# Optimization experiments

Hardware: AMD Instinct MI355X
Metric: run time of the kernel (lower is better)

The kernel has to match this reference:

```python
import jax, jax.numpy as jnp
import numpy as np

B, S, D, H = 2, 2048, 1024, 16
DK = D // H


def setup_inputs() -> dict:
    key = jax.random.key(0)
    ks = jax.random.split(key, 7)
    q = jax.random.normal(ks[0], (B, S, D), dtype=jnp.float32)
    k = jax.random.normal(ks[1], (B, S, D), dtype=jnp.float32)
    v = jax.random.normal(ks[2], (B, S, D), dtype=jnp.float32)
    # causal mask (1 = keep, 0 = mask) broadcast over batch/heads
    mask = jnp.tril(jnp.ones((S, S), dtype=jnp.int32))[None, None, :, :]
    scale = 1.0 / np.sqrt(DK)
    W_q = jax.random.normal(ks[3], (D, D), dtype=jnp.float32) * 0.02
    W_k = jax.random.normal(ks[4], (D, D), dtype=jnp.float32) * 0.02
    W_v = jax.random.normal(ks[5], (D, D), dtype=jnp.float32) * 0.02
    W_o = jax.random.normal(ks[6], (D, D), dtype=jnp.float32) * 0.02
    return {"q": q, "k": k, "v": v, "mask": mask,
            "W_q": W_q, "W_k": W_k, "W_v": W_v, "W_o": W_o}


def _split_heads(x):
    # [B, S, D] -> [B, H, S, DK]
    b, s, _ = x.shape
    return x.reshape(b, s, H, DK).transpose(0, 2, 1, 3)


def reference(q, k, v, mask, W_q, W_k, W_v, W_o):
    # nn.Linear(bias=False): y = x @ W.T
    qh = _split_heads(q @ W_q.T)
    kh = _split_heads(k @ W_k.T)
    vh = _split_heads(v @ W_v.T)
    scores = jnp.einsum("bhqd,bhkd->bhqk", qh, kh) / np.sqrt(DK)
    scores = jnp.where(mask == 0, jnp.float32(-1e9), scores)
    attn = jax.nn.softmax(scores, axis=-1)  # dropout p=0 -> identity
    out = jnp.einsum("bhqk,bhkd->bhqd", attn, vh)
    out = out.transpose(0, 2, 1, 3).reshape(q.shape[0], q.shape[1], D)
    return out @ W_o.T
```

## Files before the change

kernel.cpp:

```cpp
#include <hip/hip_runtime.h>
#include <stdint.h>
#include <stddef.h>

typedef __bf16 bf16;
typedef __attribute__((ext_vector_type(4))) __bf16 bf16x4;
typedef __attribute__((ext_vector_type(8))) __bf16 bf16x8;
typedef __attribute__((ext_vector_type(4))) float floatx4;

#define NB 2
#define NS 2048
#define ND 1024
#define NH 16
#define NDK 64
#define NBH (NB*NH)
#define NBS (NB*NS)

__device__ inline void gl2lds16(const void* g, void* l) {
  __builtin_amdgcn_global_load_lds(
      (const __attribute__((address_space(1))) uint32_t*)(const uint32_t*)g,
      (__attribute__((address_space(3))) uint32_t*)(uint32_t*)l,
      16, 0, 0);
}

__global__ __launch_bounds__(256)
void convert_w3(const float* __restrict__ Wq, const float* __restrict__ Wk,
                const float* __restrict__ Wv, bf16* __restrict__ Wb)
{
  const int z = blockIdx.y;
  const float* src = (z == 0) ? Wq : (z == 1) ? Wk : Wv;
  bf16* dst = Wb + (size_t)z * (ND * ND);
  const size_t off = ((size_t)blockIdx.x * 256 + threadIdx.x) * 32;
#pragma unroll
  for (int c = 0; c < 2; c++) {
    bf16x8 o[2];
#pragma unroll
    for (int h = 0; h < 2; h++) {
      const float4 a = *(const float4*)(src + off + c * 16 + h * 8);
      const float4 b = *(const float4*)(src + off + c * 16 + h * 8 + 4);
      o[h][0] = (bf16)a.x; o[h][1] = (bf16)a.y; o[h][2] = (bf16)a.z; o[h][3] = (bf16)a.w;
      o[h][4] = (bf16)b.x; o[h][5] = (bf16)b.y; o[h][6] = (bf16)b.z; o[h][7] = (bf16)b.w;
    }
    *(bf16x8*)(dst + off + c * 16) = o[0];
    *(bf16x8*)(dst + off + c * 16 + 8) = o[1];
  }
}

__global__ __launch_bounds__(256)
void convert_w1(const float* __restrict__ src, bf16* __restrict__ dst)
{
  const size_t off = ((size_t)blockIdx.x * 256 + threadIdx.x) * 32;
#pragma unroll
  for (int c = 0; c < 2; c++) {
    bf16x8 o[2];
#pragma unroll
    for (int h = 0; h < 2; h++) {
      const float4 a = *(const float4*)(src + off + c * 16 + h * 8);
      const float4 b = *(const float4*)(src + off + c * 16 + h * 8 + 4);
      o[h][0] = (bf16)a.x; o[h][1] = (bf16)a.y; o[h][2] = (bf16)a.z; o[h][3] = (bf16)a.w;
      o[h][4] = (bf16)b.x; o[h][5] = (bf16)b.y; o[h][6] = (bf16)b.z; o[h][7] = (bf16)b.w;
    }
    *(bf16x8*)(dst + off + c * 16) = o[0];
    *(bf16x8*)(dst + off + c * 16 + 8) = o[1];
  }
}

__global__ __launch_bounds__(256)
void proj_gemm(const float* __restrict__ q, const float* __restrict__ k,
               const float* __restrict__ v, const bf16* __restrict__ Wb,
               bf16* __restrict__ Qh, bf16* __restrict__ Kh,
               bf16* __restrict__ Vt)
{
  const int z = blockIdx.y, bx = blockIdx.x;
  const int tid = threadIdx.x;
  const int wave = tid >> 6, lane = tid & 63;
  const int quad = lane >> 4, l15 = lane & 15;

  const float* X = (z == 0) ? q : (z == 1) ? k : v;
  const bf16* W = Wb + (size_t)z * (ND * ND);
  const int c = bx & 7, r = bx >> 3;
  const int m0 = (c * 4 + (r >> 3)) * 128, n0 = (r & 7) * 128;

  __shared__ float Af[2][128 * 32];
  __shared__ bf16  Bs[2][128 * 32];

  const int wm = (wave >> 1) * 64, wn = (wave & 1) * 64;

  floatx4 acc[4][4];
#pragma unroll
  for (int i = 0; i < 4; i++)
#pragma unroll
    for (int j = 0; j < 4; j++) acc[i][j] = (floatx4)(0.0f);

  auto stage = [&](int kt, int buf) {
    const int k0 = kt * 32;
#pragma unroll
    for (int it = 0; it < 4; it++) {
      const int lin = it * 256 + tid;
      const int row = lin >> 3, slot = lin & 7;
      const int srcCh = slot ^ (row & 7);
      gl2lds16(X + (size_t)(m0 + row) * ND + k0 + srcCh * 4,
               Af[buf] + row * 32 + slot * 4);
    }
#pragma unroll
    for (int it = 0; it < 2; it++) {
      const int lin = it * 256 + tid;
      const int row = lin >> 2, ch = lin & 3;
      gl2lds16(W + (size_t)(n0 + row) * ND + k0 + ch * 8,
               Bs[buf] + lin * 8);
    }
  };

  stage(0, 0);
  for (int kk = 0; kk < 32; kk++) {
    const int cur = kk & 1;
    __builtin_amdgcn_s_waitcnt(0);
    __syncthreads();
    if (kk + 1 < 32) stage(kk + 1, cur ^ 1);

    bf16x8 af[4], bfr[4];
#pragma unroll
    for (int i = 0; i < 4; i++) {
      const int rl = wm + i * 16 + l15, r7 = rl & 7;
      const float* Ab = Af[cur] + rl * 32;
      const float4 p0 = *(const float4*)(Ab + (((2 * quad) ^ r7) << 2));
      const float4 p1 = *(const float4*)(Ab + (((2 * quad + 1) ^ r7) << 2));
      bf16x8 a;
      a[0] = (bf16)p0.x; a[1] = (bf16)p0.y; a[2] = (bf16)p0.z; a[3] = (bf16)p0.w;
      a[4] = (bf16)p1.x; a[5] = (bf16)p1.y; a[6] = (bf16)p1.z; a[7] = (bf16)p1.w;
      af[i] = a;
    }
#pragma unroll
    for (int j = 0; j < 4; j++)
      bfr[j] = *(const bf16x8*)(Bs[cur] + (wn + j * 16 + l15) * 32 + quad * 8);
#pragma unroll
    for (int i = 0; i < 4; i++)
#pragma unroll
      for (int j = 0; j < 4; j++)
        acc[i][j] = __builtin_amdgcn_mfma_f32_16x16x32_bf16(af[i], bfr[j],
                                                            acc[i][j], 0, 0, 0);
  }

  bf16* O = (z == 0) ? Qh : (z == 1) ? Kh : Vt;
#pragma unroll
  for (int i = 0; i < 4; i++) {
    const int rowb = m0 + wm + i * 16 + quad * 4;
#pragma unroll
    for (int j = 0; j < 4; j++) {
      const int col = n0 + wn + j * 16 + l15;
#pragma unroll
      for (int rr = 0; rr < 4; rr++) {
        const int row = rowb + rr;
        const bf16 o = (bf16)acc[i][j][rr];
        const int b = row >> 11, s = row & 2047;
        const int h = col >> 6,  dk = col & 63;
        if (z < 2)
          O[(((size_t)(b * NH + h)) * NS + s) * NDK + dk] = o;
        else
          O[(((size_t)(b * NH + h)) * NDK + dk) * NS + s] = o;
      }
    }
  }
}

__global__ __launch_bounds__(256)
void attn_fwd(const bf16* __restrict__ Qh, const bf16* __restrict__ Kh,
              const bf16* __restrict__ Vt, bf16* __restrict__ Ctx)
{
  const int x = blockIdx.x, bh = blockIdx.y;
  const int tid = threadIdx.x, wave = tid >> 6, lane = tid & 63;
  const int quad = lane >> 4, l15 = lane & 15;

  __shared__ bf16 Ks[2][64 * 64];
  __shared__ bf16 Vs[2][64 * 64];
  __shared__ bf16 Ps[4][16 * 64];

  const size_t qkb = (size_t)bh * NS * NDK;
  const size_t vb  = (size_t)bh * NDK * NS;
  const int b = bh >> 4, h = bh & 15;
  const float C = 0.125f * 1.44269504088896f;

  auto stage = [&](int kt, int buf) {
#pragma unroll
    for (int it = 0; it < 2; it++) {
      const int lin = it * 256 + tid;
      const int row = lin >> 3;
      const int chS = (lin & 7) ^ (row & 7);
      gl2lds16(Kh + qkb + (size_t)(kt * 64 + row) * NDK + chS * 8,
               Ks[buf] + lin * 8);
      gl2lds16(Vt + vb + (size_t)row * NS + kt * 64 + chS * 8,
               Vs[buf] + lin * 8);
    }
  };

  for (int ph = 0; ph < 2; ph++) {
    const int qt = ph ? x : 31 - x;
    const int qrow0 = qt * 64 + wave * 16;

    bf16x8 qf0, qf1;
    {
      const bf16* qp = Qh + qkb + (size_t)(qrow0 + l15) * NDK + quad * 8;
      qf0 = *(const bf16x8*)qp;
      qf1 = *(const bf16x8*)(qp + 32);
    }

    float lsum[4] = {0.0f, 0.0f, 0.0f, 0.0f};
    floatx4 oacc[4];
#pragma unroll
    for (int j = 0; j < 4; j++) oacc[j] = (floatx4)(0.0f);

    __syncthreads();
    stage(0, 0);

    for (int kt = 0; kt <= qt; kt++) {
      const int cur = kt & 1;
      __builtin_amdgcn_s_waitcnt(0);
      __syncthreads();
      if (kt < qt) stage(kt + 1, cur ^ 1);

      const bf16* Ksb = Ks[cur];
      const bf16* Vsb = Vs[cur];

      floatx4 sa[4];
#pragma unroll
      for (int jt = 0; jt < 4; jt++) {
        const int rr = jt * 16 + l15;
        const bf16x8 kf0 = *(const bf16x8*)(Ksb + rr * 64 + ((quad ^ (rr & 7)) << 3));
        const bf16x8 kf1 = *(const bf16x8*)(Ksb + rr * 64 + (((4 + quad) ^ (rr & 7)) << 3));
        floatx4 zz = (floatx4)(0.0f);
        zz = __builtin_amdgcn_mfma_f32_16x16x32_bf16(qf0, kf0, zz, 0, 0, 0);
        zz = __builtin_amdgcn_mfma_f32_16x16x32_bf16(qf1, kf1, zz, 0, 0, 0);
        sa[jt] = zz;
      }

      const bool diag = (kt == qt);
#pragma unroll
      for (int jt = 0; jt < 4; jt++) {
        const int col = jt * 16 + l15;
#pragma unroll
        for (int rr = 0; rr < 4; rr++) {
          const int row = quad * 4 + rr;
          float p = exp2f(sa[jt][rr] * C);
          if (diag) p = (kt * 64 + col <= qrow0 + row) ? p : 0.0f;
          lsum[rr] += p;
          Ps[wave][row * 64 + ((((col >> 3) ^ (row & 7))) << 3) + (col & 7)] =
              (bf16)p;
        }
      }

#pragma unroll
      for (int ks = 0; ks < 2; ks++) {
        const bf16x8 pf = *(const bf16x8*)(
            &Ps[wave][l15 * 64 + (((ks * 4 + quad) ^ (l15 & 7)) << 3)]);
#pragma unroll
        for (int jt = 0; jt < 4; jt++) {
          const int rr = jt * 16 + l15;
          const bf16x8 vf = *(const bf16x8*)(
              Vsb + rr * 64 + (((ks * 4 + quad) ^ (rr & 7)) << 3));
          oacc[jt] = __builtin_amdgcn_mfma_f32_16x16x32_bf16(pf, vf,
                                                             oacc[jt], 0, 0, 0);
        }
      }
    }

#pragma unroll
    for (int off = 1; off < 16; off <<= 1)
#pragma unroll
      for (int rr = 0; rr < 4; rr++) lsum[rr] += __shfl_xor(lsum[rr], off, 64);

#pragma unroll
    for (int jt = 0; jt < 4; jt++)
#pragma unroll
      for (int rr = 0; rr < 4; rr++) {
        const int srow = qrow0 + quad * 4 + rr;
        Ctx[((size_t)b * NS + srow) * ND + h * 64 + jt * 16 + l15] =
            (bf16)(oacc[jt][rr] / lsum[rr]);
      }
  }
}

__global__ __launch_bounds__(256)
void out_gemm(const bf16* __restrict__ Ctx, const bf16* __restrict__ WoB,
              float* __restrict__ out)
{
  const int bx = blockIdx.x, tid = threadIdx.x;
  const int wave = tid >> 6, lane = tid & 63;
  const int quad = lane >> 4, l15 = lane & 15;
  const int c = bx & 7, r = bx >> 3;
  const int m0 = (c * 8 + (r >> 3)) * 64, n0 = (r & 7) * 128;
  const int wm = (wave & 1) * 32, wn = (wave >> 1) * 64;

  __shared__ bf16 As[2][64 * 32];
  __shared__ bf16 Bs[2][128 * 32];

  floatx4 acc[2][4];
#pragma unroll
  for (int i = 0; i < 2; i++)
#pragma unroll
    for (int j = 0; j < 4; j++) acc[i][j] = (floatx4)(0.0f);

  auto stage = [&](int kt, int buf) {
    const int k0 = kt * 32;
    {
      const int row = tid >> 2, ch = tid & 3;
      gl2lds16(Ctx + (size_t)(m0 + row) * ND + k0 + ch * 8, As[buf] + tid * 8);
    }
#pragma unroll
    for (int it = 0; it < 2; it++) {
      const int lin = it * 256 + tid;
      const int row = lin >> 2, ch = lin & 3;
      gl2lds16(WoB + (size_t)(n0 + row) * ND + k0 + ch * 8, Bs[buf] + lin * 8);
    }
  };

  stage(0, 0);
  for (int kk = 0; kk < 32; kk++) {
    const int cur = kk & 1;
    __builtin_amdgcn_s_waitcnt(0);
    __syncthreads();
    if (kk + 1 < 32) stage(kk + 1, cur ^ 1);

    bf16x8 af[2], bfr[4];
#pragma unroll
    for (int i = 0; i < 2; i++)
      af[i] = *(const bf16x8*)(As[cur] + (wm + i * 16 + l15) * 32 + quad * 8);
#pragma unroll
    for (int j = 0; j < 4; j++)
      bfr[j] = *(const bf16x8*)(Bs[cur] + (wn + j * 16 + l15) * 32 + quad * 8);
#pragma unroll
    for (int i = 0; i < 2; i++)
#pragma unroll
      for (int j = 0; j < 4; j++)
        acc[i][j] = __builtin_amdgcn_mfma_f32_16x16x32_bf16(af[i], bfr[j],
                                                            acc[i][j], 0, 0, 0);
  }

#pragma unroll
  for (int i = 0; i < 2; i++) {
    const int rowb = m0 + wm + i * 16 + quad * 4;
#pragma unroll
    for (int j = 0; j < 4; j++) {
      const int col = n0 + wn + j * 16 + l15;
#pragma unroll
      for (int rr = 0; rr < 4; rr++)
        out[(size_t)(rowb + rr) * ND + col] = acc[i][j][rr];
    }
  }
}

extern "C" void kernel_launch(void* const* d_in, const int* in_sizes, int n_in,
                              void* d_out, int out_size, void* d_ws, size_t ws_size,
                              hipStream_t stream) {
  const float* q  = (const float*)d_in[0];
  const float* k  = (const float*)d_in[1];
  const float* v  = (const float*)d_in[2];
  const float* Wq = (const float*)d_in[4];
  const float* Wk = (const float*)d_in[5];
  const float* Wv = (const float*)d_in[6];
  const float* Wo = (const float*)d_in[7];
  float* out = (float*)d_out;

  const size_t elems = (size_t)NBS * ND;
  bf16* Qh  = (bf16*)d_ws;
  bf16* Kh  = Qh + elems;
  bf16* Vt  = Kh + elems;
  bf16* Ctx = Vt + elems;
  bf16* Wb  = Ctx;
  bf16* WoB = Vt;

  dim3 blk(256);
  convert_w3<<<dim3(128, 3), blk, 0, stream>>>(Wq, Wk, Wv, Wb);
  proj_gemm<<<dim3(256, 3), blk, 0, stream>>>(q, k, v, Wb, Qh, Kh, Vt);
  attn_fwd<<<dim3(16, NBH), blk, 0, stream>>>(Qh, Kh, Vt, Ctx);
  convert_w1<<<dim3(128), blk, 0, stream>>>(Wo, WoB);
  out_gemm<<<dim3(512), blk, 0, stream>>>(Ctx, WoB, out);
}
```

Before: 285.0 us.

## Replace direct global-to-LDS loads with register-staged prefetch in projection and output GEMMs

```diff
diff --git a/kernel.cpp b/kernel.cpp
--- a/kernel.cpp
+++ b/kernel.cpp
@@ -80,8 +80,11 @@
   const int c = bx & 7, r = bx >> 3;
   const int m0 = (c * 4 + (r >> 3)) * 128, n0 = (r & 7) * 128;
 
-  __shared__ float Af[2][128 * 32];
-  __shared__ bf16  Bs[2][128 * 32];
+  __shared__ bf16 As[128 * 32];
+  __shared__ bf16 Bs[128 * 32];
+
+  const int arow = tid >> 3, ach = tid & 7;
+  const int brow = tid >> 1, bch = tid & 1;
 
   const int wm = (wave >> 1) * 64, wn = (wave & 1) * 64;
 
@@ -91,47 +94,54 @@
 #pragma unroll
     for (int j = 0; j < 4; j++) acc[i][j] = (floatx4)(0.0f);
 
-  auto stage = [&](int kt, int buf) {
+  float4 ra[2][4];
+  bf16x8 rb[2];
+
+  auto loadA = [&](int kt, int p) {
     const int k0 = kt * 32;
 #pragma unroll
+    for (int it = 0; it < 4; it++)
+      ra[p][it] = *(const float4*)(X + (size_t)(m0 + it * 32 + arow) * ND + k0 + ach * 4);
+  };
+  auto loadB = [&](int kt) {
+    const int k0 = kt * 32;
+#pragma unroll
+    for (int it = 0; it < 2; it++) {
+      const int lin = it * 256 + tid;
+      const int row = lin >> 2, ch = lin & 3;
+      rb[it] = *(const bf16x8*)(W + (size_t)(n0 + row) * ND + k0 + ch * 8);
+    }
+  };
+
+  loadA(0, 0); loadB(0); loadA(1, 1);
+
+  for (int kk = 0; kk < 32; kk++) {
+    const int p = kk & 1;
+    __syncthreads();
+#pragma unroll
     for (int it = 0; it < 4; it++) {
-      const int lin = it * 256 + tid;
-      const int row = lin >> 3, slot = lin & 7;
-      const int srcCh = slot ^ (row & 7);
-      gl2lds16(X + (size_t)(m0 + row) * ND + k0 + srcCh * 4,
-               Af[buf] + row * 32 + slot * 4);
+      bf16x4 a;
+      a[0] = (bf16)ra[p][it].x; a[1] = (bf16)ra[p][it].y;
+      a[2] = (bf16)ra[p][it].z; a[3] = (bf16)ra[p][it].w;
+      *(bf16x4*)(As + (it * 32 + arow) * 32 + ach * 4) = a;
     }
 #pragma unroll
     for (int it = 0; it < 2; it++) {
       const int lin = it * 256 + tid;
       const int row = lin >> 2, ch = lin & 3;
-      gl2lds16(W + (size_t)(n0 + row) * ND + k0 + ch * 8,
-               Bs[buf] + lin * 8);
-    }
-  };
-
-  stage(0, 0);
-  for (int kk = 0; kk < 32; kk++) {
-    const int cur = kk & 1;
-    __builtin_amdgcn_s_waitcnt(0);
-    __syncthreads();
-    if (kk + 1 < 32) stage(kk + 1, cur ^ 1);
+      *(bf16x8*)(Bs + row * 32 + ch * 8) = rb[it];
+    }
+    __syncthreads();
+    if (kk + 2 < 32) loadA(kk + 2, p);
+    if (kk + 1 < 32) loadB(kk + 1);
 
     bf16x8 af[4], bfr[4];
 #pragma unroll
-    for (int i = 0; i < 4; i++) {
-      const int rl = wm + i * 16 + l15, r7 = rl & 7;
-      const float* Ab = Af[cur] + rl * 32;
-      const float4 p0 = *(const float4*)(Ab + (((2 * quad) ^ r7) << 2));
-      const float4 p1 = *(const float4*)(Ab + (((2 * quad + 1) ^ r7) << 2));
-      bf16x8 a;
-      a[0] = (bf16)p0.x; a[1] = (bf16)p0.y; a[2] = (bf16)p0.z; a[3] = (bf16)p0.w;
-      a[4] = (bf16)p1.x; a[5] = (bf16)p1.y; a[6] = (bf16)p1.z; a[7] = (bf16)p1.w;
-      af[i] = a;
-    }
+    for (int i = 0; i < 4; i++)
+      af[i] = *(const bf16x8*)(As + (wm + i * 16 + l15) * 32 + quad * 8);
 #pragma unroll
     for (int j = 0; j < 4; j++)
-      bfr[j] = *(const bf16x8*)(Bs[cur] + (wn + j * 16 + l15) * 32 + quad * 8);
+      bfr[j] = *(const bf16x8*)(Bs + (wn + j * 16 + l15) * 32 + quad * 8);
 #pragma unroll
     for (int i = 0; i < 4; i++)
 #pragma unroll
@@ -289,8 +299,10 @@
   const int m0 = (c * 8 + (r >> 3)) * 64, n0 = (r & 7) * 128;
   const int wm = (wave & 1) * 32, wn = (wave >> 1) * 64;
 
-  __shared__ bf16 As[2][64 * 32];
-  __shared__ bf16 Bs[2][128 * 32];
+  __shared__ bf16 As[64 * 32];
+  __shared__ bf16 Bs[128 * 32];
+
+  const int arow = tid >> 2, ach = tid & 3;
 
   floatx4 acc[2][4];
 #pragma unroll
@@ -298,34 +310,44 @@
 #pragma unroll
     for (int j = 0; j < 4; j++) acc[i][j] = (floatx4)(0.0f);
 
-  auto stage = [&](int kt, int buf) {
-    const int k0 = kt * 32;
-    {
-      const int row = tid >> 2, ch = tid & 3;
-      gl2lds16(Ctx + (size_t)(m0 + row) * ND + k0 + ch * 8, As[buf] + tid * 8);
-    }
+  bf16x8 raq[2];
+  bf16x8 rb[2];
+
+  auto loadA = [&](int kt, int p) {
+    raq[p] = *(const bf16x8*)(Ctx + (size_t)(m0 + arow) * ND + kt * 32 + ach * 8);
+  };
+  auto loadB = [&](int kt) {
 #pragma unroll
     for (int it = 0; it < 2; it++) {
       const int lin = it * 256 + tid;
       const int row = lin >> 2, ch = lin & 3;
-      gl2lds16(WoB + (size_t)(n0 + row) * ND + k0 + ch * 8, Bs[buf] + lin * 8);
-    }
-  };
-
-  stage(0, 0);
+      rb[it] = *(const bf16x8*)(WoB + (size_t)(n0 + row) * ND + kt * 32 + ch * 8);
+    }
+  };
+
+  loadA(0, 0); loadB(0); loadA(1, 1);
+
   for (int kk = 0; kk < 32; kk++) {
-    const int cur = kk & 1;
-    __builtin_amdgcn_s_waitcnt(0);
-    __syncthreads();
-    if (kk + 1 < 32) stage(kk + 1, cur ^ 1);
+    const int p = kk & 1;
+    __syncthreads();
+    *(bf16x8*)(As + arow * 32 + ach * 8) = raq[p];
+#pragma unroll
+    for (int it = 0; it < 2; it++) {
+      const int lin = it * 256 + tid;
+      const int row = lin >> 2, ch = lin & 3;
+      *(bf16x8*)(Bs + row * 32 + ch * 8) = rb[it];
+    }
+    __syncthreads();
+    if (kk + 2 < 32) loadA(kk + 2, p);
+    if (kk + 1 < 32) loadB(kk + 1);
 
     bf16x8 af[2], bfr[4];
 #pragma unroll
     for (int i = 0; i < 2; i++)
-      af[i] = *(const bf16x8*)(As[cur] + (wm + i * 16 + l15) * 32 + quad * 8);
+      af[i] = *(const bf16x8*)(As + (wm + i * 16 + l15) * 32 + quad * 8);
 #pragma unroll
     for (int j = 0; j < 4; j++)
-      bfr[j] = *(const bf16x8*)(Bs[cur] + (wn + j * 16 + l15) * 32 + quad * 8);
+      bfr[j] = *(const bf16x8*)(Bs + (wn + j * 16 + l15) * 32 + quad * 8);
 #pragma unroll
     for (int i = 0; i < 2; i++)
 #pragma unroll
```

New measurement: 397.2 us. 1.39x slower.
